# Performance work log

Hardware: AMD Instinct MI355X
Metric: run time of the kernel (lower is better)

The kernel has to match this reference:

```python
import jax, jax.numpy as jnp
import numpy as np

B, T, H, V = 256, 200, 256, 50000


def setup_inputs() -> dict:
    key = jax.random.key(0)
    ks = jax.random.split(key, 6)
    input_ids = jax.random.randint(ks[0], (B, T), 0, V, dtype=jnp.int64)
    lengths = jax.random.randint(ks[1], (B,), 1, T + 1, dtype=jnp.int32)
    scale = 1.0 / np.sqrt(H)
    emb = jax.random.normal(ks[2], (V + 1, H), dtype=jnp.float32) * 0.05
    w_ih = jax.random.normal(ks[3], (H, 3 * H), dtype=jnp.float32) * scale
    w_hh = jax.random.normal(ks[4], (H, 3 * H), dtype=jnp.float32) * scale
    b_ih = jnp.zeros((3 * H,), dtype=jnp.float32)
    b_hh = jnp.zeros((3 * H,), dtype=jnp.float32)
    return {"input_ids": input_ids, "lengths": lengths, "emb": emb,
            "w_ih": w_ih, "w_hh": w_hh, "b_ih": b_ih, "b_hh": b_hh}


def reference(input_ids, lengths, emb, w_ih, w_hh, b_ih, b_hh):
    # Embedding lookup: [B, T, H]
    x = emb[input_ids]
    # Precompute input-side gates for all timesteps: [B, T, 3H]
    gates_x = x @ w_ih + b_ih
    gates_x = jnp.moveaxis(gates_x, 1, 0)          # [T, B, 3H]
    t_idx = jnp.arange(T, dtype=lengths.dtype)
    mask = (t_idx[:, None] < lengths[None, :])[:, :, None]  # [T, B, 1]

    h0 = jnp.zeros((input_ids.shape[0], emb.shape[1]), dtype=emb.dtype)

    def step(h, inp):
        gx, m = inp
        rec = h @ w_hh + b_hh                       # [B, 3H] (reset_after=True)
        xz, xr, xh = jnp.split(gx, 3, axis=-1)
        rz, rr, rh = jnp.split(rec, 3, axis=-1)
        z = jax.nn.sigmoid(xz + rz)
        r = jax.nn.sigmoid(xr + rr)
        hh = jnp.tanh(xh + r * rh)
        h_new = z * h + (1.0 - z) * hh
        h = jnp.where(m, h_new, h)                  # skip padded timesteps
        return h, None

    h_final, _ = jax.lax.scan(step, h0, (gates_x, mask))
    logits = h_final @ emb.T                        # tied-embedding output: [B, V+1]
    return logits
```

## Files before the change

### kernel.cpp

```cpp
#include <hip/hip_runtime.h>
#include <hip/hip_fp16.h>

#define B_ 256
#define T_ 200
#define H_ 256
#define G3 768
#define NV 50001
#define KP 128

typedef _Float16 half2v __attribute__((ext_vector_type(2)));
typedef _Float16 half4v __attribute__((ext_vector_type(4)));
typedef _Float16 half8v __attribute__((ext_vector_type(8)));
typedef float f32x4 __attribute__((ext_vector_type(4)));

union U32H2 { unsigned int u; half2v h; };

__device__ __forceinline__ float fdot2(half2v a, half2v b, float c) {
  return __builtin_amdgcn_fdot2(a, b, c, false);
}
__device__ __forceinline__ float sigmoidf_(float x) {
  return 1.f / (1.f + __expf(-x));
}
__device__ __forceinline__ float tanhf_(float x) {
  float ax = fabsf(x);
  float e = __expf(-2.f * ax);
  float t = (1.f - e) / (1.f + e);
  return copysignf(t, x);
}
__device__ __forceinline__ f32x4 mfma16(half8v a, half8v b, f32x4 c) {
  return __builtin_amdgcn_mfma_f32_16x16x32_f16(a, b, c, 0, 0, 0);
}

__global__ __launch_bounds__(256) void pack_whh(
    const float* __restrict__ whh, unsigned int* __restrict__ out) {
  int idx = blockIdx.x * 256 + threadIdx.x;
  int p = idx / G3;
  int col = idx - p * G3;
  U32H2 u;
  u.h.x = (_Float16)whh[(size_t)(2 * p) * G3 + col];
  u.h.y = (_Float16)whh[(size_t)(2 * p + 1) * G3 + col];
  out[idx] = u.u;
}

__global__ __launch_bounds__(256) void pack_wiht(
    const float* __restrict__ wih, unsigned int* __restrict__ out) {
  int idx = blockIdx.x * 256 + threadIdx.x;
  int col = idx >> 7;
  int kk = (idx & 127) * 2;
  U32H2 u;
  u.h.x = (_Float16)wih[(size_t)kk * G3 + col];
  u.h.y = (_Float16)wih[(size_t)(kk + 1) * G3 + col];
  out[idx] = u.u;
}

__global__ __launch_bounds__(512) void gates_mfma(
    const int* __restrict__ ids, const float* __restrict__ emb,
    const __half* __restrict__ wih_t, const float* __restrict__ b_ih,
    __half* __restrict__ gates) {
  __shared__ __align__(16) _Float16 As[128 * 72];
  __shared__ __align__(16) _Float16 Bs[256 * 72];
  __shared__ int ids_s[128];
  __shared__ float bs[256];
  const int tid = threadIdx.x;
  const int r0 = blockIdx.x * 128;
  const int c0 = blockIdx.y * 256;
  const int w = tid >> 6, lane = tid & 63;
  const int wm = w >> 2, wn = w & 3;
  const int lr = lane & 15, lk = lane >> 4;

  if (tid < 128) ids_s[tid] = ids[r0 + tid];
  if (tid < 256) bs[tid] = b_ih[c0 + tid];
  __syncthreads();

  f32x4 acc[4][4];
#pragma unroll
  for (int i = 0; i < 4; ++i)
#pragma unroll
    for (int j = 0; j < 4; ++j) acc[i][j] = (f32x4){0.f, 0.f, 0.f, 0.f};

  for (int c = 0; c < 4; ++c) {
    const int kc = c * 64;
#pragma unroll
    for (int r4 = 0; r4 < 4; ++r4) {
      int q = tid + r4 * 512;
      int row = q >> 4;
      int kk = (q & 15) * 4;
      const float4 v = *(const float4*)&emb[(size_t)ids_s[row] * H_ + kc + kk];
      half4v hv = {(_Float16)v.x, (_Float16)v.y, (_Float16)v.z, (_Float16)v.w};
      *(half4v*)&As[row * 72 + kk] = hv;
    }
#pragma unroll
    for (int r4 = 0; r4 < 4; ++r4) {
      int q = tid + r4 * 512;
      int col = q >> 3;
      int cc = q & 7;
      uint4 v = *(const uint4*)((const unsigned short*)wih_t +
                                (size_t)(c0 + col) * H_ + kc + cc * 8);
      *(uint4*)&Bs[col * 72 + cc * 8] = v;
    }
    __syncthreads();
#pragma unroll
    for (int ks = 0; ks < 2; ++ks) {
      half8v af[4], bf[4];
#pragma unroll
      for (int i = 0; i < 4; ++i)
        af[i] = *(const half8v*)&As[(wm * 64 + i * 16 + lr) * 72 + ks * 32 + lk * 8];
#pragma unroll
      for (int j = 0; j < 4; ++j)
        bf[j] = *(const half8v*)&Bs[(wn * 64 + j * 16 + lr) * 72 + ks * 32 + lk * 8];
#pragma unroll
      for (int i = 0; i < 4; ++i)
#pragma unroll
        for (int j = 0; j < 4; ++j)
          acc[i][j] = mfma16(af[i], bf[j], acc[i][j]);
    }
    __syncthreads();
  }
#pragma unroll
  for (int j = 0; j < 4; ++j) {
    const int col = c0 + wn * 64 + j * 16 + lr;
    const float bj = bs[wn * 64 + j * 16 + lr];
#pragma unroll
    for (int i = 0; i < 4; ++i) {
      const int row = r0 + wm * 64 + i * 16 + lk * 4;
#pragma unroll
      for (int r = 0; r < 4; ++r)
        gates[(size_t)(row + r) * G3 + col] = (__half)(acc[i][j][r] + bj);
    }
  }
}

__device__ __forceinline__ void load_w768(const unsigned int* __restrict__ wp,
                                          int col, half2v W[KP]) {
#pragma unroll
  for (int p = 0; p < KP; ++p) {
    U32H2 u;
    u.u = wp[(size_t)p * G3 + col];
    W[p] = u.h;
  }
}

__device__ __forceinline__ float dot768(const half2v (&W)[KP],
                                        const unsigned int* __restrict__ x) {
  float a0 = 0.f, a1 = 0.f;
#pragma unroll
  for (int p4 = 0; p4 < KP / 4; ++p4) {
    uint4 v = ((const uint4*)x)[p4];
    U32H2 c0, c1, c2, c3;
    c0.u = v.x; c1.u = v.y; c2.u = v.z; c3.u = v.w;
    a0 = fdot2(W[4 * p4 + 0], c0.h, a0);
    a1 = fdot2(W[4 * p4 + 1], c1.h, a1);
    a0 = fdot2(W[4 * p4 + 2], c2.h, a0);
    a1 = fdot2(W[4 * p4 + 3], c3.h, a1);
  }
  return a0 + a1;
}

__global__ __launch_bounds__(768, 3) void rec_kernel(
    const int* __restrict__ lens, const unsigned int* __restrict__ whh_p,
    const float* __restrict__ b_hh, const __half* __restrict__ gates,
    float* __restrict__ hfin) {
  __shared__ float rec[G3];
  __shared__ __half hpk[256];
  const int tid = threadIdx.x;
  const int b = blockIdx.x;

  half2v W[KP];
  load_w768(whh_p, tid, W);

  const int len = lens[b];
  float bh0 = 0.f, bh1 = 0.f, bh2 = 0.f;
  float h = 0.f;
  if (tid < 256) {
    bh0 = b_hh[tid];
    bh1 = b_hh[256 + tid];
    bh2 = b_hh[512 + tid];
    hpk[tid] = (__half)0.f;
  }
  __syncthreads();

  const __half* gp = gates + (size_t)b * T_ * G3 + tid;
  for (int t = 0; t < len; ++t) {
    float gxz = 0.f, gxr = 0.f, gxh = 0.f;
    if (tid < 256) {
      const __half* gpt = gp + (size_t)t * G3;
      gxz = (float)gpt[0];
      gxr = (float)gpt[256];
      gxh = (float)gpt[512];
    }
    float d = dot768(W, (const unsigned int*)&hpk[0]);
    rec[tid] = d;
    __syncthreads();
    if (tid < 256) {
      float z = sigmoidf_(gxz + rec[tid] + bh0);
      float r = sigmoidf_(gxr + rec[256 + tid] + bh1);
      float hh = tanhf_(gxh + r * (rec[512 + tid] + bh2));
      h = z * h + (1.f - z) * hh;
      hpk[tid] = (__half)h;
    }
    __syncthreads();
  }
  if (tid < 256) hfin[(size_t)b * H_ + tid] = h;
}

__global__ __launch_bounds__(512) void logits_mfma(
    const float* __restrict__ hfin, const float* __restrict__ emb,
    float* __restrict__ out) {
  __shared__ __align__(16) _Float16 As[256 * 72];
  __shared__ __align__(16) _Float16 Bs[64 * 72];
  const int tid = threadIdx.x;
  const int n0 = blockIdx.x * 64;
  const int w = tid >> 6, lane = tid & 63;
  const int wm = w >> 1, wn = w & 1;
  const int lr = lane & 15, lk = lane >> 4;

  f32x4 a1[4][2], a2[4][2];
#pragma unroll
  for (int i = 0; i < 4; ++i)
#pragma unroll
    for (int j = 0; j < 2; ++j) {
      a1[i][j] = (f32x4){0.f, 0.f, 0.f, 0.f};
      a2[i][j] = (f32x4){0.f, 0.f, 0.f, 0.f};
    }

  for (int c = 0; c < 8; ++c) {
    const int kc = c * 32;
#pragma unroll
    for (int r4 = 0; r4 < 4; ++r4) {
      int q = tid + r4 * 512;
      int row = q >> 3;
      int kk = (q & 7) * 4;
      float4 v = *(const float4*)&hfin[(size_t)row * H_ + kc + kk];
      half4v hi = {(_Float16)v.x, (_Float16)v.y, (_Float16)v.z, (_Float16)v.w};
      half4v lo = {(_Float16)((v.x - (float)hi.x) * 1024.f),
                   (_Float16)((v.y - (float)hi.y) * 1024.f),
                   (_Float16)((v.z - (float)hi.z) * 1024.f),
                   (_Float16)((v.w - (float)hi.w) * 1024.f)};
      int base = row * 72 + (kk >> 3) * 16 + (kk & 7);
      *(half4v*)&As[base] = hi;
      *(half4v*)&As[base + 8] = lo;
    }
    {
      int col = tid >> 3;
      int kk = (tid & 7) * 4;
      int n = n0 + col;
      float4 v = (n < NV) ? *(const float4*)&emb[(size_t)n * H_ + kc + kk]
                          : make_float4(0.f, 0.f, 0.f, 0.f);
      half4v hi = {(_Float16)v.x, (_Float16)v.y, (_Float16)v.z, (_Float16)v.w};
      half4v lo = {(_Float16)((v.x - (float)hi.x) * 1024.f),
                   (_Float16)((v.y - (float)hi.y) * 1024.f),
                   (_Float16)((v.z - (float)hi.z) * 1024.f),
                   (_Float16)((v.w - (float)hi.w) * 1024.f)};
      int base = col * 72 + (kk >> 3) * 16 + (kk & 7);
      *(half4v*)&Bs[base] = hi;
      *(half4v*)&Bs[base + 8] = lo;
    }
    __syncthreads();
    half8v ah[4], al[4];
#pragma unroll
    for (int i = 0; i < 4; ++i) {
      int base = (wm * 64 + i * 16 + lr) * 72 + lk * 16;
      ah[i] = *(const half8v*)&As[base];
      al[i] = *(const half8v*)&As[base + 8];
    }
#pragma unroll
    for (int j = 0; j < 2; ++j) {
      int base = (wn * 32 + j * 16 + lr) * 72 + lk * 16;
      half8v bh = *(const half8v*)&Bs[base];
      half8v bl = *(const half8v*)&Bs[base + 8];
#pragma unroll
      for (int i = 0; i < 4; ++i) {
        a1[i][j] = mfma16(ah[i], bh, a1[i][j]);
        a2[i][j] = mfma16(ah[i], bl, a2[i][j]);
        a2[i][j] = mfma16(al[i], bh, a2[i][j]);
      }
    }
    __syncthreads();
  }
#pragma unroll
  for (int j = 0; j < 2; ++j) {
    int n = n0 + wn * 32 + j * 16 + lr;
    if (n < NV) {
#pragma unroll
      for (int i = 0; i < 4; ++i) {
        int row = wm * 64 + i * 16 + lk * 4;
#pragma unroll
        for (int r = 0; r < 4; ++r)
          out[(size_t)(row + r) * NV + n] =
              a1[i][j][r] + a2[i][j][r] * (1.f / 1024.f);
      }
    }
  }
}

extern "C" void kernel_launch(void* const* d_in, const int* in_sizes, int n_in,
                              void* d_out, int out_size, void* d_ws, size_t ws_size,
                              hipStream_t stream) {
  const int* ids = (const int*)d_in[0];
  const int* lens = (const int*)d_in[1];
  const float* emb = (const float*)d_in[2];
  const float* w_ih = (const float*)d_in[3];
  const float* w_hh = (const float*)d_in[4];
  const float* b_ih = (const float*)d_in[5];
  const float* b_hh = (const float*)d_in[6];
  float* out = (float*)d_out;

  char* ws = (char*)d_ws;
  __half* gates = (__half*)ws;
  float* hfin = (float*)(ws + (size_t)B_ * T_ * G3 * sizeof(__half));
  unsigned int* whh_p =
      (unsigned int*)(ws + (size_t)B_ * T_ * G3 * sizeof(__half)
                      + (size_t)B_ * H_ * sizeof(float));
  unsigned int* wih_t = whh_p + (size_t)KP * G3;

  pack_whh<<<dim3(384), dim3(256), 0, stream>>>(w_hh, whh_p);
  pack_wiht<<<dim3(384), dim3(256), 0, stream>>>(w_ih, wih_t);
  gates_mfma<<<dim3(400, 3), dim3(512), 0, stream>>>(
      ids, emb, (const __half*)wih_t, b_ih, gates);
  rec_kernel<<<dim3(B_), dim3(768), 0, stream>>>(lens, whh_p, b_hh, gates, hfin);
  logits_mfma<<<dim3((NV + 63) / 64), dim3(512), 0, stream>>>(hfin, emb, out);
}
```

Before: 438.6 us.

## Batch GRU recurrence over 16 sequences per block using MFMA

New measurement: 888.7 us. +102.6%, slower.

```diff
diff --git a/kernel.cpp b/kernel.cpp
--- a/kernel.cpp
+++ b/kernel.cpp
@@ -6,7 +6,6 @@
 #define H_ 256
 #define G3 768
 #define NV 50001
-#define KP 128
 
 typedef _Float16 half2v __attribute__((ext_vector_type(2)));
 typedef _Float16 half4v __attribute__((ext_vector_type(4)));
@@ -15,9 +14,6 @@
 
 union U32H2 { unsigned int u; half2v h; };
 
-__device__ __forceinline__ float fdot2(half2v a, half2v b, float c) {
-  return __builtin_amdgcn_fdot2(a, b, c, false);
-}
 __device__ __forceinline__ float sigmoidf_(float x) {
   return 1.f / (1.f + __expf(-x));
 }
@@ -31,14 +27,19 @@
   return __builtin_amdgcn_mfma_f32_16x16x32_f16(a, b, c, 0, 0, 0);
 }
 
-__global__ __launch_bounds__(256) void pack_whh(
+__global__ __launch_bounds__(256) void pack_whh_frag(
     const float* __restrict__ whh, unsigned int* __restrict__ out) {
   int idx = blockIdx.x * 256 + threadIdx.x;
-  int p = idx / G3;
-  int col = idx - p * G3;
+  int f = idx >> 8;
+  int rem = idx & 255;
+  int lane = rem >> 2;
+  int jp = rem & 3;
+  int nt = f >> 3, kc = f & 7;
+  int col = nt * 16 + (lane & 15);
+  int k = kc * 32 + (lane >> 4) * 8 + jp * 2;
   U32H2 u;
-  u.h.x = (_Float16)whh[(size_t)(2 * p) * G3 + col];
-  u.h.y = (_Float16)whh[(size_t)(2 * p + 1) * G3 + col];
+  u.h.x = (_Float16)whh[(size_t)k * G3 + col];
+  u.h.y = (_Float16)whh[(size_t)(k + 1) * G3 + col];
   out[idx] = u.u;
 }
 
@@ -62,13 +63,14 @@
   __shared__ int ids_s[128];
   __shared__ float bs[256];
   const int tid = threadIdx.x;
-  const int r0 = blockIdx.x * 128;
+  const int t = blockIdx.x >> 1;
+  const int bbase0 = (blockIdx.x & 1) * 128;
   const int c0 = blockIdx.y * 256;
   const int w = tid >> 6, lane = tid & 63;
   const int wm = w >> 2, wn = w & 3;
   const int lr = lane & 15, lk = lane >> 4;
 
-  if (tid < 128) ids_s[tid] = ids[r0 + tid];
+  if (tid < 128) ids_s[tid] = ids[(bbase0 + tid) * T_ + t];
   if (tid < 256) bs[tid] = b_ih[c0 + tid];
   __syncthreads();
 
@@ -116,91 +118,149 @@
     }
     __syncthreads();
   }
+  const int bgb = (bbase0 + wm * 64) >> 4;
 #pragma unroll
   for (int j = 0; j < 4; ++j) {
     const int col = c0 + wn * 64 + j * 16 + lr;
     const float bj = bs[wn * 64 + j * 16 + lr];
 #pragma unroll
     for (int i = 0; i < 4; ++i) {
-      const int row = r0 + wm * 64 + i * 16 + lk * 4;
+      size_t base = ((size_t)((t * 16 + bgb + i) * 768 + col)) * 16 + lk * 4;
+      half4v hv = {(_Float16)(acc[i][j][0] + bj), (_Float16)(acc[i][j][1] + bj),
+                   (_Float16)(acc[i][j][2] + bj), (_Float16)(acc[i][j][3] + bj)};
+      *(half4v*)&gates[base] = hv;
+    }
+  }
+}
+
+__global__ __launch_bounds__(512, 2) __attribute__((amdgpu_waves_per_eu(2, 2)))
+void rec_mfma(const int* __restrict__ lens,
+              const unsigned int* __restrict__ whh_f,
+              const float* __restrict__ b_hh,
+              const __half* __restrict__ gates, float* __restrict__ hfin) {
+  __shared__ _Float16 h_lds[16 * 264];
+  __shared__ __align__(16) unsigned int Bw[24576];
+  const int tid = threadIdx.x;
+  const int bg = blockIdx.x;
+  const int w = tid >> 6, lane = tid & 63;
+  const int lr = lane & 15, lk = lane >> 4;
+
+  half8v Wr[3][2][6];
+#pragma unroll
+  for (int g = 0; g < 3; ++g)
+#pragma unroll
+    for (int cb = 0; cb < 2; ++cb) {
+      int nt = g * 16 + w * 2 + cb;
+#pragma unroll
+      for (int kc = 0; kc < 6; ++kc) {
+        uint4 v = *(const uint4*)&whh_f[((nt * 8 + kc) * 64 + lane) * 4];
+        Wr[g][cb][kc] = __builtin_bit_cast(half8v, v);
+      }
+    }
+#pragma unroll
+  for (int g = 0; g < 3; ++g)
+#pragma unroll
+    for (int cb = 0; cb < 2; ++cb)
+#pragma unroll
+      for (int kc = 0; kc < 6; ++kc)
+        asm volatile("" : "+v"(Wr[g][cb][kc]));
+
+#pragma unroll
+  for (int p = 0; p < 6; ++p)
+#pragma unroll
+    for (int q = 0; q < 2; ++q) {
+      int g = p >> 1, cb = p & 1;
+      int nt = g * 16 + w * 2 + cb;
+      uint4 v = *(const uint4*)&whh_f[((nt * 8 + 6 + q) * 64 + lane) * 4];
+      *(uint4*)&Bw[(((w * 6 + p) * 2 + q) * 64 + lane) * 4] = v;
+    }
+  for (int i = tid; i < 16 * 132; i += 512) ((unsigned int*)h_lds)[i] = 0;
+
+  int len_r[4];
+#pragma unroll
+  for (int r = 0; r < 4; ++r) len_r[r] = lens[bg * 16 + lk * 4 + r];
+  int lmax = 0;
+  for (int i = 0; i < 16; ++i) lmax = max(lmax, lens[bg * 16 + i]);
+
+  float bhh[3][2];
+  int goff[3][2];
+#pragma unroll
+  for (int g = 0; g < 3; ++g)
+#pragma unroll
+    for (int cb = 0; cb < 2; ++cb) {
+      int col = g * 256 + w * 32 + cb * 16 + lr;
+      bhh[g][cb] = b_hh[col];
+      goff[g][cb] = col * 16 + lk * 4;
+    }
+  float h_old[2][4];
+#pragma unroll
+  for (int cb = 0; cb < 2; ++cb)
+#pragma unroll
+    for (int r = 0; r < 4; ++r) h_old[cb][r] = 0.f;
+  __syncthreads();
+
+  const __half* gbase = gates + (size_t)bg * 12288;
+  for (int t = 0; t < lmax; ++t) {
+    const __half* gt = gbase + (size_t)t * 196608;
+    half4v gx[3][2];
+#pragma unroll
+    for (int g = 0; g < 3; ++g)
+#pragma unroll
+      for (int cb = 0; cb < 2; ++cb)
+        gx[g][cb] = *(const half4v*)(gt + goff[g][cb]);
+
+    f32x4 acc[3][2];
+#pragma unroll
+    for (int g = 0; g < 3; ++g)
+#pragma unroll
+      for (int cb = 0; cb < 2; ++cb)
+        acc[g][cb] = (f32x4){bhh[g][cb], bhh[g][cb], bhh[g][cb], bhh[g][cb]};
+
+#pragma unroll
+    for (int kc = 0; kc < 6; ++kc) {
+      half8v a = *(const half8v*)&h_lds[lr * 264 + kc * 32 + lk * 8];
+#pragma unroll
+      for (int g = 0; g < 3; ++g)
+#pragma unroll
+        for (int cb = 0; cb < 2; ++cb)
+          acc[g][cb] = mfma16(a, Wr[g][cb][kc], acc[g][cb]);
+    }
+#pragma unroll
+    for (int q = 0; q < 2; ++q) {
+      half8v a = *(const half8v*)&h_lds[lr * 264 + (6 + q) * 32 + lk * 8];
+#pragma unroll
+      for (int p = 0; p < 6; ++p) {
+        int g = p >> 1, cb = p & 1;
+        half8v bw = *(const half8v*)&Bw[(((w * 6 + p) * 2 + q) * 64 + lane) * 4];
+        acc[g][cb] = mfma16(a, bw, acc[g][cb]);
+      }
+    }
+#pragma unroll
+    for (int cb = 0; cb < 2; ++cb)
+#pragma unroll
+      for (int r = 0; r < 4; ++r) {
+        float z = sigmoidf_((float)gx[0][cb][r] + acc[0][cb][r]);
+        float rr = sigmoidf_((float)gx[1][cb][r] + acc[1][cb][r]);
+        float hh = tanhf_((float)gx[2][cb][r] + rr * acc[2][cb][r]);
+        float hv = z * h_old[cb][r] + (1.f - z) * hh;
+        if (t < len_r[r]) h_old[cb][r] = hv;
+      }
+    __syncthreads();
+#pragma unroll
+    for (int cb = 0; cb < 2; ++cb) {
+      int colh = w * 32 + cb * 16 + lr;
 #pragma unroll
       for (int r = 0; r < 4; ++r)
-        gates[(size_t)(row + r) * G3 + col] = (__half)(acc[i][j][r] + bj);
-    }
-  }
-}
-
-__device__ __forceinline__ void load_w768(const unsigned int* __restrict__ wp,
-                                          int col, half2v W[KP]) {
-#pragma unroll
-  for (int p = 0; p < KP; ++p) {
-    U32H2 u;
-    u.u = wp[(size_t)p * G3 + col];
-    W[p] = u.h;
-  }
-}
-
-__device__ __forceinline__ float dot768(const half2v (&W)[KP],
-                                        const unsigned int* __restrict__ x) {
-  float a0 = 0.f, a1 = 0.f;
-#pragma unroll
-  for (int p4 = 0; p4 < KP / 4; ++p4) {
-    uint4 v = ((const uint4*)x)[p4];
-    U32H2 c0, c1, c2, c3;
-    c0.u = v.x; c1.u = v.y; c2.u = v.z; c3.u = v.w;
-    a0 = fdot2(W[4 * p4 + 0], c0.h, a0);
-    a1 = fdot2(W[4 * p4 + 1], c1.h, a1);
-    a0 = fdot2(W[4 * p4 + 2], c2.h, a0);
-    a1 = fdot2(W[4 * p4 + 3], c3.h, a1);
-  }
-  return a0 + a1;
-}
-
-__global__ __launch_bounds__(768, 3) void rec_kernel(
-    const int* __restrict__ lens, const unsigned int* __restrict__ whh_p,
-    const float* __restrict__ b_hh, const __half* __restrict__ gates,
-    float* __restrict__ hfin) {
-  __shared__ float rec[G3];
-  __shared__ __half hpk[256];
-  const int tid = threadIdx.x;
-  const int b = blockIdx.x;
-
-  half2v W[KP];
-  load_w768(whh_p, tid, W);
-
-  const int len = lens[b];
-  float bh0 = 0.f, bh1 = 0.f, bh2 = 0.f;
-  float h = 0.f;
-  if (tid < 256) {
-    bh0 = b_hh[tid];
-    bh1 = b_hh[256 + tid];
-    bh2 = b_hh[512 + tid];
-    hpk[tid] = (__half)0.f;
-  }
-  __syncthreads();
-
-  const __half* gp = gates + (size_t)b * T_ * G3 + tid;
-  for (int t = 0; t < len; ++t) {
-    float gxz = 0.f, gxr = 0.f, gxh = 0.f;
-    if (tid < 256) {
-      const __half* gpt = gp + (size_t)t * G3;
-      gxz = (float)gpt[0];
-      gxr = (float)gpt[256];
-      gxh = (float)gpt[512];
-    }
-    float d = dot768(W, (const unsigned int*)&hpk[0]);
-    rec[tid] = d;
-    __syncthreads();
-    if (tid < 256) {
-      float z = sigmoidf_(gxz + rec[tid] + bh0);
-      float r = sigmoidf_(gxr + rec[256 + tid] + bh1);
-      float hh = tanhf_(gxh + r * (rec[512 + tid] + bh2));
-      h = z * h + (1.f - z) * hh;
-      hpk[tid] = (__half)h;
-    }
-    __syncthreads();
-  }
-  if (tid < 256) hfin[(size_t)b * H_ + tid] = h;
+        h_lds[(lk * 4 + r) * 264 + colh] = (_Float16)h_old[cb][r];
+    }
+    __syncthreads();
+  }
+#pragma unroll
+  for (int cb = 0; cb < 2; ++cb)
+#pragma unroll
+    for (int r = 0; r < 4; ++r)
+      hfin[(size_t)(bg * 16 + lk * 4 + r) * H_ + w * 32 + cb * 16 + lr] =
+          h_old[cb][r];
 }
 
 __global__ __launch_bounds__(512) void logits_mfma(
@@ -308,15 +368,15 @@
   char* ws = (char*)d_ws;
   __half* gates = (__half*)ws;
   float* hfin = (float*)(ws + (size_t)B_ * T_ * G3 * sizeof(__half));
-  unsigned int* whh_p =
+  unsigned int* whh_f =
       (unsigned int*)(ws + (size_t)B_ * T_ * G3 * sizeof(__half)
                       + (size_t)B_ * H_ * sizeof(float));
-  unsigned int* wih_t = whh_p + (size_t)KP * G3;
-
-  pack_whh<<<dim3(384), dim3(256), 0, stream>>>(w_hh, whh_p);
+  unsigned int* wih_t = whh_f + (size_t)98304;
+
+  pack_whh_frag<<<dim3(384), dim3(256), 0, stream>>>(w_hh, whh_f);
   pack_wiht<<<dim3(384), dim3(256), 0, stream>>>(w_ih, wih_t);
   gates_mfma<<<dim3(400, 3), dim3(512), 0, stream>>>(
       ids, emb, (const __half*)wih_t, b_ih, gates);
-  rec_kernel<<<dim3(B_), dim3(768), 0, stream>>>(lens, whh_p, b_hh, gates, hfin);
+  rec_mfma<<<dim3(16), dim3(512), 0, stream>>>(lens, whh_f, b_hh, gates, hfin);
   logits_mfma<<<dim3((NV + 63) / 64), dim3(512), 0, stream>>>(hfin, emb, out);
 }
```

## Split recurrent weights between registers and LDS to cut register pressure

Applied to the files above, without the earlier changes.

New measurement: 468.0 us. 6.7% more time.

```diff
diff --git a/kernel.cpp b/kernel.cpp
--- a/kernel.cpp
+++ b/kernel.cpp
@@ -6,7 +6,8 @@
 #define H_ 256
 #define G3 768
 #define NV 50001
-#define KP 128
+#define RQ 20
+#define LQ 12
 
 typedef _Float16 half2v __attribute__((ext_vector_type(2)));
 typedef _Float16 half4v __attribute__((ext_vector_type(4)));
@@ -30,15 +31,30 @@
 __device__ __forceinline__ f32x4 mfma16(half8v a, half8v b, f32x4 c) {
   return __builtin_amdgcn_mfma_f32_16x16x32_f16(a, b, c, 0, 0, 0);
 }
-
-__global__ __launch_bounds__(256) void pack_whh(
+__device__ __forceinline__ float dot4u(uint4 w, uint4 h, float a0, float a1,
+                                       float* o1) {
+  U32H2 w0, w1, w2, w3, c0, c1, c2, c3;
+  w0.u = w.x; w1.u = w.y; w2.u = w.z; w3.u = w.w;
+  c0.u = h.x; c1.u = h.y; c2.u = h.z; c3.u = h.w;
+  a0 = fdot2(w0.h, c0.h, a0);
+  a1 = fdot2(w1.h, c1.h, a1);
+  a0 = fdot2(w2.h, c2.h, a0);
+  a1 = fdot2(w3.h, c3.h, a1);
+  *o1 = a1;
+  return a0;
+}
+
+__global__ __launch_bounds__(256) void pack_whh_r(
     const float* __restrict__ whh, unsigned int* __restrict__ out) {
   int idx = blockIdx.x * 256 + threadIdx.x;
-  int p = idx / G3;
-  int col = idx - p * G3;
+  int j = idx & 3;
+  int e = idx >> 2;
+  int q = e / G3;
+  int col = e - q * G3;
+  int k = 2 * (4 * q + j);
   U32H2 u;
-  u.h.x = (_Float16)whh[(size_t)(2 * p) * G3 + col];
-  u.h.y = (_Float16)whh[(size_t)(2 * p + 1) * G3 + col];
+  u.h.x = (_Float16)whh[(size_t)k * G3 + col];
+  u.h.y = (_Float16)whh[(size_t)(k + 1) * G3 + col];
   out[idx] = u.u;
 }
 
@@ -130,43 +146,31 @@
   }
 }
 
-__device__ __forceinline__ void load_w768(const unsigned int* __restrict__ wp,
-                                          int col, half2v W[KP]) {
-#pragma unroll
-  for (int p = 0; p < KP; ++p) {
-    U32H2 u;
-    u.u = wp[(size_t)p * G3 + col];
-    W[p] = u.h;
-  }
-}
-
-__device__ __forceinline__ float dot768(const half2v (&W)[KP],
-                                        const unsigned int* __restrict__ x) {
-  float a0 = 0.f, a1 = 0.f;
-#pragma unroll
-  for (int p4 = 0; p4 < KP / 4; ++p4) {
-    uint4 v = ((const uint4*)x)[p4];
-    U32H2 c0, c1, c2, c3;
-    c0.u = v.x; c1.u = v.y; c2.u = v.z; c3.u = v.w;
-    a0 = fdot2(W[4 * p4 + 0], c0.h, a0);
-    a1 = fdot2(W[4 * p4 + 1], c1.h, a1);
-    a0 = fdot2(W[4 * p4 + 2], c2.h, a0);
-    a1 = fdot2(W[4 * p4 + 3], c3.h, a1);
-  }
-  return a0 + a1;
-}
-
-__global__ __launch_bounds__(768, 3) void rec_kernel(
-    const int* __restrict__ lens, const unsigned int* __restrict__ whh_p,
-    const float* __restrict__ b_hh, const __half* __restrict__ gates,
-    float* __restrict__ hfin) {
+__global__ __launch_bounds__(768, 3) __attribute__((amdgpu_waves_per_eu(3, 3)))
+void rec_kernel(const int* __restrict__ lens,
+                const unsigned int* __restrict__ whh_r,
+                const float* __restrict__ b_hh, const __half* __restrict__ gates,
+                float* __restrict__ hfin) {
   __shared__ float rec[G3];
-  __shared__ __half hpk[256];
+  __shared__ __align__(16) __half hpk[256];
+  __shared__ uint4 Wl4[LQ * G3];
   const int tid = threadIdx.x;
   const int b = blockIdx.x;
 
-  half2v W[KP];
-  load_w768(whh_p, tid, W);
+  const uint4* wr = (const uint4*)whh_r + tid;
+  uint4 Wv[RQ];
+#pragma unroll
+  for (int q = 0; q < RQ; ++q) {
+    asm volatile("global_load_dwordx4 %0, %1, off"
+                 : "=v"(Wv[q])
+                 : "v"(wr + (size_t)q * G3));
+  }
+  asm volatile("s_waitcnt vmcnt(0)" ::: "memory");
+  __builtin_amdgcn_sched_barrier(0);
+
+#pragma unroll
+  for (int q = 0; q < LQ; ++q)
+    Wl4[q * G3 + tid] = wr[(size_t)(RQ + q) * G3];
 
   const int len = lens[b];
   float bh0 = 0.f, bh1 = 0.f, bh2 = 0.f;
@@ -179,6 +183,7 @@
   }
   __syncthreads();
 
+  const uint4* hx = (const uint4*)&hpk[0];
   const __half* gp = gates + (size_t)b * T_ * G3 + tid;
   for (int t = 0; t < len; ++t) {
     float gxz = 0.f, gxr = 0.f, gxh = 0.f;
@@ -188,8 +193,16 @@
       gxr = (float)gpt[256];
       gxh = (float)gpt[512];
     }
-    float d = dot768(W, (const unsigned int*)&hpk[0]);
-    rec[tid] = d;
+    float a0 = 0.f, a1 = 0.f;
+#pragma unroll
+    for (int q = 0; q < RQ; ++q)
+      a0 = dot4u(Wv[q], hx[q], a0, a1, &a1);
+#pragma unroll
+    for (int q = 0; q < LQ; ++q) {
+      uint4 wv = Wl4[q * G3 + tid];
+      a0 = dot4u(wv, hx[RQ + q], a0, a1, &a1);
+    }
+    rec[tid] = a0 + a1;
     __syncthreads();
     if (tid < 256) {
       float z = sigmoidf_(gxz + rec[tid] + bh0);
@@ -308,15 +321,15 @@
   char* ws = (char*)d_ws;
   __half* gates = (__half*)ws;
   float* hfin = (float*)(ws + (size_t)B_ * T_ * G3 * sizeof(__half));
-  unsigned int* whh_p =
+  unsigned int* whh_r =
       (unsigned int*)(ws + (size_t)B_ * T_ * G3 * sizeof(__half)
                       + (size_t)B_ * H_ * sizeof(float));
-  unsigned int* wih_t = whh_p + (size_t)KP * G3;
-
-  pack_whh<<<dim3(384), dim3(256), 0, stream>>>(w_hh, whh_p);
+  unsigned int* wih_t = whh_r + (size_t)98304;
+
+  pack_whh_r<<<dim3(384), dim3(256), 0, stream>>>(w_hh, whh_r);
   pack_wiht<<<dim3(384), dim3(256), 0, stream>>>(w_ih, wih_t);
   gates_mfma<<<dim3(400, 3), dim3(512), 0, stream>>>(
       ids, emb, (const __half*)wih_t, b_ih, gates);
-  rec_kernel<<<dim3(B_), dim3(768), 0, stream>>>(lens, whh_p, b_hh, gates, hfin);
+  rec_kernel<<<dim3(B_), dim3(768), 0, stream>>>(lens, whh_r, b_hh, gates, hfin);
   logits_mfma<<<dim3((NV + 63) / 64), dim3(512), 0, stream>>>(hfin, emb, out);
 }
```
